# Kernel optimization log

Hardware: AMD Instinct MI355X
Metric: run time of the kernel (lower is better)

Reference implementation:

```python
import jax, jax.numpy as jnp
import numpy as np

D_MODEL = 768
N_HEADS = 12
HEAD_DIM = D_MODEL // N_HEADS


def setup_inputs() -> dict:
    key = jax.random.key(0)
    ks = jax.random.split(key, 9)
    s = 0.02
    B, S = 16, 1024
    return {
        "x": jax.random.normal(ks[0], (B, S, D_MODEL), dtype=jnp.float32),
        "Wq": jax.random.normal(ks[1], (D_MODEL, D_MODEL), dtype=jnp.float32) * s,
        "bq": jnp.zeros((D_MODEL,), dtype=jnp.float32),
        "Wk": jax.random.normal(ks[2], (D_MODEL, D_MODEL), dtype=jnp.float32) * s,
        "bk": jnp.zeros((D_MODEL,), dtype=jnp.float32),
        "Wv": jax.random.normal(ks[3], (D_MODEL, D_MODEL), dtype=jnp.float32) * s,
        "bv": jnp.zeros((D_MODEL,), dtype=jnp.float32),
        "Wc": jax.random.normal(ks[4], (D_MODEL, D_MODEL), dtype=jnp.float32) * s,
        "bc": jnpp if False else jnp.zeros((D_MODEL,), dtype=jnp.float32),
    }


def _split_heads(t):
    # [B, S, D] -> [B, H, S, Dh]
    B, S, _ = t.shape
    return t.reshape(B, S, N_HEADS, HEAD_DIM).transpose(0, 2, 1, 3)


def reference(x, Wq, bq, Wk, bk, Wv, bv, Wc, bc):
    # nn.Linear: y = x @ W.T + b ; here W stored as [out, in]-equivalent square
    q = _split_heads(x @ Wq.T + bq)
    k = _split_heads(x @ Wk.T + bk)
    v = _split_heads(x @ Wv.T + bv)
    scale = jnp.asarray(HEAD_DIM, x.dtype) ** 0.5
    scores = jnp.einsum("bhsd,bhtd->bhst", q, k) / scale  # [B,H,S,S]
    attn = jax.nn.softmax(scores, axis=-1)
    # dropout omitted (deterministic / inference-mode reference)
    ctx = jnp.einsum("bhst,bhtd->bhsd", attn, v)  # [B,H,S,Dh]
    B, H, S, Dh = ctx.shape
    ctx = ctx.transpose(0, 2, 1, 3).reshape(B, S, H * Dh)
    return ctx @ Wc.T + bc
```

## Files before the change

kernel.cpp:

```cpp
#include <hip/hip_runtime.h>
#include <hip/hip_bf16.h>
#include <stdint.h>

#define D_MODEL 768
#define NHEADS 12
#define HDIM 64
#define BATCH 16
#define SEQ 1024
#define MTOK (BATCH*SEQ)
#define LOG2E 1.4426950408889634f

typedef __bf16 bfrag  __attribute__((ext_vector_type(8)));
typedef __bf16 bf16x4 __attribute__((ext_vector_type(4)));
typedef float  f32x4  __attribute__((ext_vector_type(4)));
typedef short  s16x4  __attribute__((ext_vector_type(4)));

__device__ __forceinline__ void gload16(const void* g, void* l) {
  __builtin_amdgcn_global_load_lds(
      (const __attribute__((address_space(1))) unsigned int*)g,
      (__attribute__((address_space(3))) unsigned int*)l, 16, 0, 0);
}

__device__ __forceinline__ float fexp2(float x) {
#if __has_builtin(__builtin_amdgcn_exp2f)
  return __builtin_amdgcn_exp2f(x);
#else
  return exp2f(x);
#endif
}

__device__ __forceinline__ void mfma16(bf16x4 a, bf16x4 b, f32x4& c) {
#if __has_builtin(__builtin_amdgcn_mfma_f32_16x16x16bf16_1k)
  c = __builtin_amdgcn_mfma_f32_16x16x16bf16_1k(
        __builtin_bit_cast(s16x4, a), __builtin_bit_cast(s16x4, b), c, 0, 0, 0);
#else
  asm volatile("s_nop 1\n\tv_mfma_f32_16x16x16_bf16 %0, %1, %2, %0\n\ts_nop 7\n\ts_nop 7"
               : "+v"(c) : "v"(a), "v"(b));
#endif
}

__global__ __launch_bounds__(256) void convert_kernel(
    const float* __restrict__ x,
    const float* __restrict__ Wq, const float* __restrict__ Wk,
    const float* __restrict__ Wv, const float* __restrict__ Wc,
    __bf16* __restrict__ xb, __bf16* __restrict__ Wb)
{
  const size_t NX = (size_t)MTOK * D_MODEL;
  const size_t NW = (size_t)D_MODEL * D_MODEL;
  size_t i = ((size_t)blockIdx.x * 256 + threadIdx.x) * 4;
  const float* src; __bf16* dst; size_t off;
  if (i < NX) { src = x; dst = xb; off = i; }
  else {
    size_t wj = i - NX;
    int which = (int)(wj / NW);
    off = wj - (size_t)which * NW;
    src = which == 0 ? Wq : which == 1 ? Wk : which == 2 ? Wv : Wc;
    dst = Wb + (size_t)which * NW;
  }
  f32x4 v = *(const f32x4*)(src + off);
  bf16x4 o;
  o[0] = (__bf16)v[0]; o[1] = (__bf16)v[1]; o[2] = (__bf16)v[2]; o[3] = (__bf16)v[3];
  *(bf16x4*)(dst + off) = o;
}

__global__ __launch_bounds__(256) void qkv_gemm(
    const __bf16* __restrict__ A,
    const __bf16* __restrict__ W,
    const float* __restrict__ bq, const float* __restrict__ bk, const float* __restrict__ bv,
    __bf16* __restrict__ Qb,
    __bf16* __restrict__ Kb,
    __bf16* __restrict__ VTb)
{
  __shared__ __bf16 As[128 * 32];
  __shared__ __bf16 Bs[128 * 32];
  const int tid = threadIdx.x;
  const int lane = tid & 63, w = tid >> 6;
  const int wm = w >> 1, wn = w & 1;
  const int bm = blockIdx.x, bn = blockIdx.y;
  const int r4 = lane >> 2, c8 = (lane & 3) << 3;
  const int l15 = lane & 15, q8 = (lane >> 4) << 3;

  f32x4 acc[4][4];
#pragma unroll
  for (int mt = 0; mt < 4; ++mt)
#pragma unroll
    for (int nt = 0; nt < 4; ++nt) acc[mt][nt] = (f32x4){0.f, 0.f, 0.f, 0.f};

  const size_t am0 = (size_t)bm * 128;
  const size_t bn0 = (size_t)bn * 128;

  for (int kt = 0; kt < 24; ++kt) {
    const int k0 = kt * 32;
#pragma unroll
    for (int i = 0; i < 2; ++i) {
      const int rr = i * 64 + w * 16;
      gload16(A + (am0 + rr + r4) * D_MODEL + k0 + c8, &As[rr * 32]);
      gload16(W + (bn0 + rr + r4) * D_MODEL + k0 + c8, &Bs[rr * 32]);
    }
    __syncthreads();
    bfrag af[4], bf[4];
#pragma unroll
    for (int t = 0; t < 4; ++t) {
      af[t] = *(const bfrag*)&As[(wm * 64 + t * 16 + l15) * 32 + q8];
      bf[t] = *(const bfrag*)&Bs[(wn * 64 + t * 16 + l15) * 32 + q8];
    }
#pragma unroll
    for (int mt = 0; mt < 4; ++mt)
#pragma unroll
      for (int nt = 0; nt < 4; ++nt)
        acc[mt][nt] = __builtin_amdgcn_mfma_f32_16x16x32_bf16(af[mt], bf[nt], acc[mt][nt], 0, 0, 0);
    __syncthreads();
  }

  const int which = bn / 6;
  const int obase = (bn % 6) * 128 + wn * 64;
  const float* bias = which == 0 ? bq : which == 1 ? bk : bv;
  const float qscale = 0.125f * LOG2E;
#pragma unroll
  for (int mt = 0; mt < 4; ++mt) {
    const int row0 = bm * 128 + wm * 64 + mt * 16 + (lane >> 4) * 4;
    const int b = row0 >> 10, s = row0 & 1023;
#pragma unroll
    for (int nt = 0; nt < 4; ++nt) {
      const int o = obase + nt * 16 + l15;
      const float bo = bias[o];
      const int h = o >> 6, d = o & 63;
      const size_t hb = ((size_t)(b * NHEADS + h)) << 16;
      if (which == 2) {
        bf16x4 pv;
#pragma unroll
        for (int r = 0; r < 4; ++r) pv[r] = (__bf16)(acc[mt][nt][r] + bo);
        const int tc = s & 63;
        const size_t addr = hb + (size_t)(s >> 6) * 4096 + (size_t)d * 64
                          + (size_t)((((tc >> 3) ^ (d & 7))) << 3) + (tc & 7);
        *(bf16x4*)&VTb[addr] = pv;
      } else if (which == 0) {
#pragma unroll
        for (int r = 0; r < 4; ++r) {
          const int sr = s + r;
          const size_t addr = hb + (size_t)sr * 64 + (size_t)(((d >> 3) ^ (sr & 7)) << 3) + (d & 7);
          Qb[addr] = (__bf16)((acc[mt][nt][r] + bo) * qscale);
        }
      } else {
#pragma unroll
        for (int r = 0; r < 4; ++r) {
          const int sr = s + r;
          const size_t addr = hb + (size_t)sr * 64 + (size_t)(((d >> 3) ^ (sr & 7)) << 3) + (d & 7);
          Kb[addr] = (__bf16)(acc[mt][nt][r] + bo);
        }
      }
    }
  }
}

__global__ __launch_bounds__(256, 3) void attn_kernel(
    const __bf16* __restrict__ Qb, const __bf16* __restrict__ Kb,
    const __bf16* __restrict__ VTb, __bf16* __restrict__ ctx)
{
  __shared__ __align__(16) char smem_raw[32768];
  __shared__ float rs[256];
  __bf16* S = (__bf16*)smem_raw;
  const int tid = threadIdx.x, lane = tid & 63, w = tid >> 6;
  const int blk = blockIdx.x;
  const int xcd = blk & 7, slot = blk >> 3;
  const int bh = xcd * 24 + (slot >> 4);
  const int qt = slot & 15;
  const int l15 = lane & 15, quad = lane >> 4;
  const int h3 = l15 & 7;
  const size_t base = (size_t)bh << 16;

  const int soff = w * 1024 + lane * 8;

  {
    const __bf16* gq = Qb + base + qt * 4096 + soff;
    const __bf16* gk = Kb + base + soff;
    const __bf16* gv = VTb + base + soff;
    gload16(gq,       S + 12288 + soff);
    gload16(gq + 512, S + 12288 + soff + 512);
    gload16(gk,       S + soff);
    gload16(gk + 512, S + soff + 512);
    gload16(gv,       S + 8192 + soff);
    gload16(gv + 512, S + 8192 + soff + 512);
  }
  __syncthreads();

  bfrag bq[4][2];
#pragma unroll
  for (int q2 = 0; q2 < 4; ++q2) {
    const int fq = 12288 + (q2 * 16 + l15) * 64 + ((quad ^ h3) << 3);
    bq[q2][0] = *(const bfrag*)&S[fq];
    bq[q2][1] = *(const bfrag*)&S[fq ^ 32];
  }
  __syncthreads();

  f32x4 Oa[4][4];
#pragma unroll
  for (int dt = 0; dt < 4; ++dt)
#pragma unroll
    for (int q2 = 0; q2 < 4; ++q2) Oa[dt][q2] = (f32x4){0.f, 0.f, 0.f, 0.f};
  float sacc[4] = {0.f, 0.f, 0.f, 0.f};

  const int fk  = (w * 16 + l15) * 64 + ((quad ^ h3) << 3);
  const int fvb = l15 * 64 + (((w * 2 + (quad >> 1)) ^ h3) << 3) + ((quad & 1) << 2);

  for (int j = 0; j < 16; ++j) {
    const int cb = j & 1, nb = cb ^ 1;
    if (j < 15) {
      const __bf16* gk = Kb + base + (j + 1) * 4096 + soff;
      const __bf16* gv = VTb + base + (j + 1) * 4096 + soff;
      gload16(gk,       S + nb * 4096 + soff);
      gload16(gk + 512, S + nb * 4096 + soff + 512);
      gload16(gv,       S + 8192 + nb * 4096 + soff);
      gload16(gv + 512, S + 8192 + nb * 4096 + soff + 512);
    }
    const __bf16* Kc = S + cb * 4096;
    const __bf16* Vc = S + 8192 + cb * 4096;

    bfrag ak0 = *(const bfrag*)&Kc[fk];
    bfrag ak1 = *(const bfrag*)&Kc[fk ^ 32];
    bf16x4 av[4];
#pragma unroll
    for (int dt = 0; dt < 4; ++dt) av[dt] = *(const bf16x4*)&Vc[dt * 1024 + fvb];

    bf16x4 pb[4];
#pragma unroll
    for (int q2 = 0; q2 < 4; ++q2) {
      f32x4 s4 = (f32x4){0.f, 0.f, 0.f, 0.f};
      s4 = __builtin_amdgcn_mfma_f32_16x16x32_bf16(ak0, bq[q2][0], s4, 0, 0, 0);
      s4 = __builtin_amdgcn_mfma_f32_16x16x32_bf16(ak1, bq[q2][1], s4, 0, 0, 0);
      const float p0 = fexp2(s4[0]), p1 = fexp2(s4[1]);
      const float p2 = fexp2(s4[2]), p3 = fexp2(s4[3]);
      sacc[q2] += (p0 + p1) + (p2 + p3);
      bf16x4 pv;
      pv[0] = (__bf16)p0; pv[1] = (__bf16)p1; pv[2] = (__bf16)p2; pv[3] = (__bf16)p3;
      pb[q2] = pv;
    }

#pragma unroll
    for (int dt = 0; dt < 4; ++dt)
#pragma unroll
      for (int q2 = 0; q2 < 4; ++q2)
        mfma16(av[dt], pb[q2], Oa[dt][q2]);

    __syncthreads();
  }

  float vsum[4];
#pragma unroll
  for (int q2 = 0; q2 < 4; ++q2) {
    float v = sacc[q2];
    v += __shfl_xor(v, 16);
    v += __shfl_xor(v, 32);
    vsum[q2] = v;
  }
  if (quad == 0) {
#pragma unroll
    for (int q2 = 0; q2 < 4; ++q2) rs[w * 64 + q2 * 16 + l15] = vsum[q2];
  }
  __syncthreads();
  if (w == 0) {
    const float tot = rs[lane] + rs[64 + lane] + rs[128 + lane] + rs[192 + lane];
    rs[lane] = 1.0f / tot;
  }
  __syncthreads();

  float* fs = (float*)smem_raw;
  const int b = bh / NHEADS, h = bh - b * NHEADS;
  const int off = l15 * 16 + quad * 4;
#pragma unroll
  for (int rd = 0; rd < 2; ++rd) {
#pragma unroll
    for (int dl = 0; dl < 2; ++dl)
#pragma unroll
      for (int q2 = 0; q2 < 4; ++q2)
        *(f32x4*)&fs[w * 2048 + dl * 1024 + q2 * 256 + off] = Oa[rd * 2 + dl][q2];
    __syncthreads();
#pragma unroll
    for (int e = 0; e < 2; ++e) {
      const int idx = w * 2 + e;
      const int dl = idx >> 2, q2 = idx & 3;
      const int tb = dl * 1024 + q2 * 256 + off;
      f32x4 s0 = *(const f32x4*)&fs[tb];
      f32x4 s1 = *(const f32x4*)&fs[2048 + tb];
      f32x4 s2 = *(const f32x4*)&fs[4096 + tb];
      f32x4 s3 = *(const f32x4*)&fs[6144 + tb];
      f32x4 sum = (s0 + s1) + (s2 + s3);
      const float li = rs[q2 * 16 + l15];
      const int dt = rd * 2 + dl;
      const int s = qt * 64 + q2 * 16 + l15;
      bf16x4 o4;
#pragma unroll
      for (int r = 0; r < 4; ++r) o4[r] = (__bf16)(sum[r] * li);
      *(bf16x4*)&ctx[((size_t)(b * SEQ + s)) * D_MODEL + h * HDIM + dt * 16 + quad * 4] = o4;
    }
    __syncthreads();
  }
}

__global__ __launch_bounds__(256) void out_gemm(
    const __bf16* __restrict__ A,
    const __bf16* __restrict__ W,
    const float* __restrict__ bc,
    float* __restrict__ out)
{
  __shared__ __bf16 As[128 * 32];
  __shared__ __bf16 Bs[128 * 32];
  const int tid = threadIdx.x;
  const int lane = tid & 63, w = tid >> 6;
  const int wm = w >> 1, wn = w & 1;
  const int bm = blockIdx.x, bn = blockIdx.y;
  const int r4 = lane >> 2, c8 = (lane & 3) << 3;
  const int l15 = lane & 15, q8 = (lane >> 4) << 3;

  f32x4 acc[4][4];
#pragma unroll
  for (int mt = 0; mt < 4; ++mt)
#pragma unroll
    for (int nt = 0; nt < 4; ++nt) acc[mt][nt] = (f32x4){0.f, 0.f, 0.f, 0.f};

  const size_t am0 = (size_t)bm * 128;
  const size_t bn0 = (size_t)bn * 128;

  for (int kt = 0; kt < 24; ++kt) {
    const int k0 = kt * 32;
#pragma unroll
    for (int i = 0; i < 2; ++i) {
      const int rr = i * 64 + w * 16;
      gload16(A + (am0 + rr + r4) * D_MODEL + k0 + c8, &As[rr * 32]);
      gload16(W + (bn0 + rr + r4) * D_MODEL + k0 + c8, &Bs[rr * 32]);
    }
    __syncthreads();
    bfrag af[4], bf[4];
#pragma unroll
    for (int t = 0; t < 4; ++t) {
      af[t] = *(const bfrag*)&As[(wm * 64 + t * 16 + l15) * 32 + q8];
      bf[t] = *(const bfrag*)&Bs[(wn * 64 + t * 16 + l15) * 32 + q8];
    }
#pragma unroll
    for (int mt = 0; mt < 4; ++mt)
#pragma unroll
      for (int nt = 0; nt < 4; ++nt)
        acc[mt][nt] = __builtin_amdgcn_mfma_f32_16x16x32_bf16(af[mt], bf[nt], acc[mt][nt], 0, 0, 0);
    __syncthreads();
  }

#pragma unroll
  for (int mt = 0; mt < 4; ++mt) {
    const int row0 = bm * 128 + wm * 64 + mt * 16 + (lane >> 4) * 4;
#pragma unroll
    for (int nt = 0; nt < 4; ++nt) {
      const int o = bn * 128 + wn * 64 + nt * 16 + l15;
      const float bo = bc[o];
#pragma unroll
      for (int r = 0; r < 4; ++r)
        out[(size_t)(row0 + r) * D_MODEL + o] = acc[mt][nt][r] + bo;
    }
  }
}

extern "C" void kernel_launch(void* const* d_in, const int* in_sizes, int n_in,
                              void* d_out, int out_size, void* d_ws, size_t ws_size,
                              hipStream_t stream)
{
  const float* x  = (const float*)d_in[0];
  const float* Wq = (const float*)d_in[1];
  const float* bq = (const float*)d_in[2];
  const float* Wk = (const float*)d_in[3];
  const float* bk = (const float*)d_in[4];
  const float* Wv = (const float*)d_in[5];
  const float* bv = (const float*)d_in[6];
  const float* Wc = (const float*)d_in[7];
  const float* bc = (const float*)d_in[8];
  float* out = (float*)d_out;

  char* ws = (char*)d_ws;
  __bf16* xb  = (__bf16*)(ws);
  __bf16* Wb  = (__bf16*)(ws + 25165824);
  __bf16* Qb  = (__bf16*)(ws + 29884416);
  __bf16* Kb  = (__bf16*)(ws + 55050240);
  __bf16* VTb = (__bf16*)(ws + 80216064);
  __bf16* ctx = xb;

  convert_kernel<<<14592, 256, 0, stream>>>(x, Wq, Wk, Wv, Wc, xb, Wb);
  qkv_gemm<<<dim3(128, 18), 256, 0, stream>>>(xb, Wb, bq, bk, bv, Qb, Kb, VTb);
  attn_kernel<<<3072, 256, 0, stream>>>(Qb, Kb, VTb, ctx);
  out_gemm<<<dim3(128, 6), 256, 0, stream>>>(ctx, Wb + 3 * 589824, bc, out);
}
```

Baseline: 290.0 us.

## Rewrite projection GEMMs with 256x256 tiles and a 4-stage async LDS pipeline

```diff
diff --git a/kernel.cpp b/kernel.cpp
--- a/kernel.cpp
+++ b/kernel.cpp
@@ -63,62 +63,81 @@
   *(bf16x4*)(dst + off) = o;
 }
 
-__global__ __launch_bounds__(256) void qkv_gemm(
+__device__ __forceinline__ void gemm256_core(
+    const __bf16* __restrict__ A, const __bf16* __restrict__ Bp,
+    int am0, int bn0, __bf16* S, f32x4 (&acc)[8][4])
+{
+  const int tid = threadIdx.x;
+  const int lane = tid & 63, w = tid >> 6;
+  const int l15 = lane & 15, quad = lane >> 4;
+  const int wm = w >> 2, wn = w & 3;
+  const size_t sA0 = (size_t)(am0 + w * 16 + l15) * D_MODEL + quad * 8;
+  const size_t sA1 = sA0 + (size_t)128 * D_MODEL;
+  const size_t sB0 = (size_t)(bn0 + w * 16 + l15) * D_MODEL + quad * 8;
+  const size_t sB1 = sB0 + (size_t)128 * D_MODEL;
+  const int d0 = tid * 8, d1 = 4096 + tid * 8;
+
+#define STG(t) { __bf16* Ls = S + ((t) & 3) * 16384; const int k0 = (t) * 32; \
+    gload16(A  + sA0 + k0, Ls + d0);        \
+    gload16(A  + sA1 + k0, Ls + d1);        \
+    gload16(Bp + sB0 + k0, Ls + 8192 + d0); \
+    gload16(Bp + sB1 + k0, Ls + 8192 + d1); }
+
+#pragma unroll
+  for (int mt = 0; mt < 8; ++mt)
+#pragma unroll
+    for (int nt = 0; nt < 4; ++nt) acc[mt][nt] = (f32x4){0.f, 0.f, 0.f, 0.f};
+
+  STG(0); STG(1); STG(2);
+  asm volatile("s_waitcnt vmcnt(8)" ::: "memory");
+  __builtin_amdgcn_s_barrier();
+
+  for (int t = 0; t < 24; ++t) {
+    if (t < 21) STG(t + 3);
+    const __bf16* As_ = S + (t & 3) * 16384;
+    const __bf16* Bs_ = As_ + 8192;
+    bfrag bfr[4];
+#pragma unroll
+    for (int nt = 0; nt < 4; ++nt)
+      bfr[nt] = *(const bfrag*)&Bs_[(wn * 4 + nt) * 512 + lane * 8];
+    __builtin_amdgcn_s_setprio(1);
+#pragma unroll
+    for (int mt = 0; mt < 8; ++mt) {
+      bfrag afr = *(const bfrag*)&As_[(wm * 8 + mt) * 512 + lane * 8];
+#pragma unroll
+      for (int nt = 0; nt < 4; ++nt)
+        acc[mt][nt] = __builtin_amdgcn_mfma_f32_16x16x32_bf16(afr, bfr[nt], acc[mt][nt], 0, 0, 0);
+    }
+    __builtin_amdgcn_s_setprio(0);
+    if (t < 21)       asm volatile("s_waitcnt vmcnt(8)" ::: "memory");
+    else if (t == 21) asm volatile("s_waitcnt vmcnt(4)" ::: "memory");
+    else if (t == 22) asm volatile("s_waitcnt vmcnt(0)" ::: "memory");
+    if (t < 23) __builtin_amdgcn_s_barrier();
+  }
+#undef STG
+}
+
+__global__ __launch_bounds__(512, 2) void qkv_gemm(
     const __bf16* __restrict__ A,
     const __bf16* __restrict__ W,
     const float* __restrict__ bq, const float* __restrict__ bk, const float* __restrict__ bv,
-    __bf16* __restrict__ Qb,
-    __bf16* __restrict__ Kb,
-    __bf16* __restrict__ VTb)
-{
-  __shared__ __bf16 As[128 * 32];
-  __shared__ __bf16 Bs[128 * 32];
-  const int tid = threadIdx.x;
-  const int lane = tid & 63, w = tid >> 6;
-  const int wm = w >> 1, wn = w & 1;
-  const int bm = blockIdx.x, bn = blockIdx.y;
-  const int r4 = lane >> 2, c8 = (lane & 3) << 3;
-  const int l15 = lane & 15, q8 = (lane >> 4) << 3;
-
-  f32x4 acc[4][4];
-#pragma unroll
-  for (int mt = 0; mt < 4; ++mt)
-#pragma unroll
-    for (int nt = 0; nt < 4; ++nt) acc[mt][nt] = (f32x4){0.f, 0.f, 0.f, 0.f};
-
-  const size_t am0 = (size_t)bm * 128;
-  const size_t bn0 = (size_t)bn * 128;
-
-  for (int kt = 0; kt < 24; ++kt) {
-    const int k0 = kt * 32;
-#pragma unroll
-    for (int i = 0; i < 2; ++i) {
-      const int rr = i * 64 + w * 16;
-      gload16(A + (am0 + rr + r4) * D_MODEL + k0 + c8, &As[rr * 32]);
-      gload16(W + (bn0 + rr + r4) * D_MODEL + k0 + c8, &Bs[rr * 32]);
-    }
-    __syncthreads();
-    bfrag af[4], bf[4];
-#pragma unroll
-    for (int t = 0; t < 4; ++t) {
-      af[t] = *(const bfrag*)&As[(wm * 64 + t * 16 + l15) * 32 + q8];
-      bf[t] = *(const bfrag*)&Bs[(wn * 64 + t * 16 + l15) * 32 + q8];
-    }
-#pragma unroll
-    for (int mt = 0; mt < 4; ++mt)
-#pragma unroll
-      for (int nt = 0; nt < 4; ++nt)
-        acc[mt][nt] = __builtin_amdgcn_mfma_f32_16x16x32_bf16(af[mt], bf[nt], acc[mt][nt], 0, 0, 0);
-    __syncthreads();
-  }
-
-  const int which = bn / 6;
-  const int obase = (bn % 6) * 128 + wn * 64;
+    __bf16* __restrict__ Qb, __bf16* __restrict__ Kb, __bf16* __restrict__ VTb)
+{
+  __shared__ __bf16 S[65536];
+  f32x4 acc[8][4];
+  const int bm = blockIdx.x & 63, bn = blockIdx.x >> 6;
+  gemm256_core(A, W, bm * 256, bn * 256, S, acc);
+
+  const int tid = threadIdx.x, lane = tid & 63, w = tid >> 6;
+  const int wm = w >> 2, wn = w & 3;
+  const int l15 = lane & 15, quad = lane >> 4;
+  const int which = bn / 3;
+  const int obase = (bn % 3) * 256 + wn * 64;
   const float* bias = which == 0 ? bq : which == 1 ? bk : bv;
   const float qscale = 0.125f * LOG2E;
 #pragma unroll
-  for (int mt = 0; mt < 4; ++mt) {
-    const int row0 = bm * 128 + wm * 64 + mt * 16 + (lane >> 4) * 4;
+  for (int mt = 0; mt < 8; ++mt) {
+    const int row0 = bm * 256 + wm * 128 + mt * 16 + quad * 4;
     const int b = row0 >> 10, s = row0 & 1023;
 #pragma unroll
     for (int nt = 0; nt < 4; ++nt) {
@@ -297,59 +316,26 @@
   }
 }
 
-__global__ __launch_bounds__(256) void out_gemm(
+__global__ __launch_bounds__(512, 2) void out_gemm(
     const __bf16* __restrict__ A,
     const __bf16* __restrict__ W,
     const float* __restrict__ bc,
     float* __restrict__ out)
 {
-  __shared__ __bf16 As[128 * 32];
-  __shared__ __bf16 Bs[128 * 32];
-  const int tid = threadIdx.x;
-  const int lane = tid & 63, w = tid >> 6;
-  const int wm = w >> 1, wn = w & 1;
-  const int bm = blockIdx.x, bn = blockIdx.y;
-  const int r4 = lane >> 2, c8 = (lane & 3) << 3;
-  const int l15 = lane & 15, q8 = (lane >> 4) << 3;
-
-  f32x4 acc[4][4];
-#pragma unroll
-  for (int mt = 0; mt < 4; ++mt)
-#pragma unroll
-    for (int nt = 0; nt < 4; ++nt) acc[mt][nt] = (f32x4){0.f, 0.f, 0.f, 0.f};
-
-  const size_t am0 = (size_t)bm * 128;
-  const size_t bn0 = (size_t)bn * 128;
-
-  for (int kt = 0; kt < 24; ++kt) {
-    const int k0 = kt * 32;
-#pragma unroll
-    for (int i = 0; i < 2; ++i) {
-      const int rr = i * 64 + w * 16;
-      gload16(A + (am0 + rr + r4) * D_MODEL + k0 + c8, &As[rr * 32]);
-      gload16(W + (bn0 + rr + r4) * D_MODEL + k0 + c8, &Bs[rr * 32]);
-    }
-    __syncthreads();
-    bfrag af[4], bf[4];
-#pragma unroll
-    for (int t = 0; t < 4; ++t) {
-      af[t] = *(const bfrag*)&As[(wm * 64 + t * 16 + l15) * 32 + q8];
-      bf[t] = *(const bfrag*)&Bs[(wn * 64 + t * 16 + l15) * 32 + q8];
-    }
-#pragma unroll
-    for (int mt = 0; mt < 4; ++mt)
-#pragma unroll
-      for (int nt = 0; nt < 4; ++nt)
-        acc[mt][nt] = __builtin_amdgcn_mfma_f32_16x16x32_bf16(af[mt], bf[nt], acc[mt][nt], 0, 0, 0);
-    __syncthreads();
-  }
-
-#pragma unroll
-  for (int mt = 0; mt < 4; ++mt) {
-    const int row0 = bm * 128 + wm * 64 + mt * 16 + (lane >> 4) * 4;
+  __shared__ __bf16 S[65536];
+  f32x4 acc[8][4];
+  const int bm = blockIdx.x & 63, bn = blockIdx.x >> 6;
+  gemm256_core(A, W, bm * 256, bn * 256, S, acc);
+
+  const int tid = threadIdx.x, lane = tid & 63, w = tid >> 6;
+  const int wm = w >> 2, wn = w & 3;
+  const int l15 = lane & 15, quad = lane >> 4;
+#pragma unroll
+  for (int mt = 0; mt < 8; ++mt) {
+    const int row0 = bm * 256 + wm * 128 + mt * 16 + quad * 4;
 #pragma unroll
     for (int nt = 0; nt < 4; ++nt) {
-      const int o = bn * 128 + wn * 64 + nt * 16 + l15;
+      const int o = bn * 256 + wn * 64 + nt * 16 + l15;
       const float bo = bc[o];
 #pragma unroll
       for (int r = 0; r < 4; ++r)
@@ -382,7 +368,7 @@
   __bf16* ctx = xb;
 
   convert_kernel<<<14592, 256, 0, stream>>>(x, Wq, Wk, Wv, Wc, xb, Wb);
-  qkv_gemm<<<dim3(128, 18), 256, 0, stream>>>(xb, Wb, bq, bk, bv, Qb, Kb, VTb);
+  qkv_gemm<<<576, 512, 0, stream>>>(xb, Wb, bq, bk, bv, Qb, Kb, VTb);
   attn_kernel<<<3072, 256, 0, stream>>>(Qb, Kb, VTb, ctx);
-  out_gemm<<<dim3(128, 6), 256, 0, stream>>>(ctx, Wb + 3 * 589824, bc, out);
-}
+  out_gemm<<<192, 512, 0, stream>>>(ctx, Wb + 3 * 589824, bc, out);
+}
```

Result: slower. 304.5 us (+5.0%).

## Process 128-key K/V tiles per attention iteration with larger LDS buffers

Applied to the files above, without the earlier changes.

```diff
diff --git a/kernel.cpp b/kernel.cpp
--- a/kernel.cpp
+++ b/kernel.cpp
@@ -67,9 +67,7 @@
     const __bf16* __restrict__ A,
     const __bf16* __restrict__ W,
     const float* __restrict__ bq, const float* __restrict__ bk, const float* __restrict__ bv,
-    __bf16* __restrict__ Qb,
-    __bf16* __restrict__ Kb,
-    __bf16* __restrict__ VTb)
+    __bf16* __restrict__ Qb, __bf16* __restrict__ Kb, __bf16* __restrict__ VTb)
 {
   __shared__ __bf16 As[128 * 32];
   __shared__ __bf16 Bs[128 * 32];
@@ -153,11 +151,11 @@
   }
 }
 
-__global__ __launch_bounds__(256, 3) void attn_kernel(
+__global__ __launch_bounds__(256, 2) void attn_kernel(
     const __bf16* __restrict__ Qb, const __bf16* __restrict__ Kb,
     const __bf16* __restrict__ VTb, __bf16* __restrict__ ctx)
 {
-  __shared__ __align__(16) char smem_raw[32768];
+  __shared__ __align__(16) char smem_raw[65536];
   __shared__ float rs[256];
   __bf16* S = (__bf16*)smem_raw;
   const int tid = threadIdx.x, lane = tid & 63, w = tid >> 6;
@@ -169,25 +167,27 @@
   const int h3 = l15 & 7;
   const size_t base = (size_t)bh << 16;
 
-  const int soff = w * 1024 + lane * 8;
+  const int soff  = w * 1024 + lane * 8;
+  const int soff2 = w * 2048 + lane * 8;
 
   {
     const __bf16* gq = Qb + base + qt * 4096 + soff;
-    const __bf16* gk = Kb + base + soff;
-    const __bf16* gv = VTb + base + soff;
-    gload16(gq,       S + 12288 + soff);
-    gload16(gq + 512, S + 12288 + soff + 512);
-    gload16(gk,       S + soff);
-    gload16(gk + 512, S + soff + 512);
-    gload16(gv,       S + 8192 + soff);
-    gload16(gv + 512, S + 8192 + soff + 512);
+    gload16(gq,       S + 24576 + soff);
+    gload16(gq + 512, S + 24576 + soff + 512);
+    const __bf16* gk = Kb + base + soff2;
+    const __bf16* gv = VTb + base + soff2;
+#pragma unroll
+    for (int c = 0; c < 4; ++c) {
+      gload16(gk + c * 512, S + soff2 + c * 512);
+      gload16(gv + c * 512, S + 16384 + soff2 + c * 512);
+    }
   }
   __syncthreads();
 
   bfrag bq[4][2];
 #pragma unroll
   for (int q2 = 0; q2 < 4; ++q2) {
-    const int fq = 12288 + (q2 * 16 + l15) * 64 + ((quad ^ h3) << 3);
+    const int fq = 24576 + (q2 * 16 + l15) * 64 + ((quad ^ h3) << 3);
     bq[q2][0] = *(const bfrag*)&S[fq];
     bq[q2][1] = *(const bfrag*)&S[fq ^ 32];
   }
@@ -200,47 +200,53 @@
     for (int q2 = 0; q2 < 4; ++q2) Oa[dt][q2] = (f32x4){0.f, 0.f, 0.f, 0.f};
   float sacc[4] = {0.f, 0.f, 0.f, 0.f};
 
-  const int fk  = (w * 16 + l15) * 64 + ((quad ^ h3) << 3);
-  const int fvb = l15 * 64 + (((w * 2 + (quad >> 1)) ^ h3) << 3) + ((quad & 1) << 2);
-
-  for (int j = 0; j < 16; ++j) {
+  for (int j = 0; j < 8; ++j) {
     const int cb = j & 1, nb = cb ^ 1;
-    if (j < 15) {
-      const __bf16* gk = Kb + base + (j + 1) * 4096 + soff;
-      const __bf16* gv = VTb + base + (j + 1) * 4096 + soff;
-      gload16(gk,       S + nb * 4096 + soff);
-      gload16(gk + 512, S + nb * 4096 + soff + 512);
-      gload16(gv,       S + 8192 + nb * 4096 + soff);
-      gload16(gv + 512, S + 8192 + nb * 4096 + soff + 512);
-    }
-    const __bf16* Kc = S + cb * 4096;
-    const __bf16* Vc = S + 8192 + cb * 4096;
-
-    bfrag ak0 = *(const bfrag*)&Kc[fk];
-    bfrag ak1 = *(const bfrag*)&Kc[fk ^ 32];
-    bf16x4 av[4];
-#pragma unroll
-    for (int dt = 0; dt < 4; ++dt) av[dt] = *(const bf16x4*)&Vc[dt * 1024 + fvb];
-
-    bf16x4 pb[4];
-#pragma unroll
-    for (int q2 = 0; q2 < 4; ++q2) {
-      f32x4 s4 = (f32x4){0.f, 0.f, 0.f, 0.f};
-      s4 = __builtin_amdgcn_mfma_f32_16x16x32_bf16(ak0, bq[q2][0], s4, 0, 0, 0);
-      s4 = __builtin_amdgcn_mfma_f32_16x16x32_bf16(ak1, bq[q2][1], s4, 0, 0, 0);
-      const float p0 = fexp2(s4[0]), p1 = fexp2(s4[1]);
-      const float p2 = fexp2(s4[2]), p3 = fexp2(s4[3]);
-      sacc[q2] += (p0 + p1) + (p2 + p3);
-      bf16x4 pv;
-      pv[0] = (__bf16)p0; pv[1] = (__bf16)p1; pv[2] = (__bf16)p2; pv[3] = (__bf16)p3;
-      pb[q2] = pv;
-    }
-
-#pragma unroll
-    for (int dt = 0; dt < 4; ++dt)
-#pragma unroll
-      for (int q2 = 0; q2 < 4; ++q2)
-        mfma16(av[dt], pb[q2], Oa[dt][q2]);
+    if (j < 7) {
+      const __bf16* gk = Kb + base + (j + 1) * 8192 + soff2;
+      const __bf16* gv = VTb + base + (j + 1) * 8192 + soff2;
+#pragma unroll
+      for (int c = 0; c < 4; ++c) {
+        gload16(gk + c * 512, S + nb * 8192 + soff2 + c * 512);
+        gload16(gv + c * 512, S + 16384 + nb * 8192 + soff2 + c * 512);
+      }
+    }
+    const __bf16* Kc = S + cb * 8192;
+    const __bf16* Vc = S + 16384 + cb * 8192;
+
+#pragma unroll
+    for (int g = 0; g < 2; ++g) {
+      const int tb = w * 32 + g * 16;
+      const int fk = (tb + l15) * 64 + ((quad ^ h3) << 3);
+      bfrag ak0 = *(const bfrag*)&Kc[fk];
+      bfrag ak1 = *(const bfrag*)&Kc[fk ^ 32];
+      const int fvb = (w >> 1) * 4096 + l15 * 64
+                    + ((((w & 1) * 4 + g * 2 + (quad >> 1)) ^ h3) << 3)
+                    + ((quad & 1) << 2);
+      bf16x4 av[4];
+#pragma unroll
+      for (int dt = 0; dt < 4; ++dt) av[dt] = *(const bf16x4*)&Vc[fvb + dt * 1024];
+
+      bf16x4 pb[4];
+#pragma unroll
+      for (int q2 = 0; q2 < 4; ++q2) {
+        f32x4 s4 = (f32x4){0.f, 0.f, 0.f, 0.f};
+        s4 = __builtin_amdgcn_mfma_f32_16x16x32_bf16(ak0, bq[q2][0], s4, 0, 0, 0);
+        s4 = __builtin_amdgcn_mfma_f32_16x16x32_bf16(ak1, bq[q2][1], s4, 0, 0, 0);
+        const float p0 = fexp2(s4[0]), p1 = fexp2(s4[1]);
+        const float p2 = fexp2(s4[2]), p3 = fexp2(s4[3]);
+        sacc[q2] += (p0 + p1) + (p2 + p3);
+        bf16x4 pv;
+        pv[0] = (__bf16)p0; pv[1] = (__bf16)p1; pv[2] = (__bf16)p2; pv[3] = (__bf16)p3;
+        pb[q2] = pv;
+      }
+
+#pragma unroll
+      for (int dt = 0; dt < 4; ++dt)
+#pragma unroll
+        for (int q2 = 0; q2 < 4; ++q2)
+          mfma16(av[dt], pb[q2], Oa[dt][q2]);
+    }
 
     __syncthreads();
   }
@@ -279,11 +285,11 @@
     for (int e = 0; e < 2; ++e) {
       const int idx = w * 2 + e;
       const int dl = idx >> 2, q2 = idx & 3;
-      const int tb = dl * 1024 + q2 * 256 + off;
-      f32x4 s0 = *(const f32x4*)&fs[tb];
-      f32x4 s1 = *(const f32x4*)&fs[2048 + tb];
-      f32x4 s2 = *(const f32x4*)&fs[4096 + tb];
-      f32x4 s3 = *(const f32x4*)&fs[6144 + tb];
+      const int tb2 = dl * 1024 + q2 * 256 + off;
+      f32x4 s0 = *(const f32x4*)&fs[tb2];
+      f32x4 s1 = *(const f32x4*)&fs[2048 + tb2];
+      f32x4 s2 = *(const f32x4*)&fs[4096 + tb2];
+      f32x4 s3 = *(const f32x4*)&fs[6144 + tb2];
       f32x4 sum = (s0 + s1) + (s2 + s3);
       const float li = rs[q2 * 16 + l15];
       const int dt = rd * 2 + dl;
```

Result: slower. 303.0 us (+4.5%).

## Deepen GEMM K-tile to 64 with XOR-swizzled LDS and pad attention reduction

Applied to the files above, without the earlier changes.

```diff
diff --git a/kernel.cpp b/kernel.cpp
--- a/kernel.cpp
+++ b/kernel.cpp
@@ -63,22 +63,23 @@
   *(bf16x4*)(dst + off) = o;
 }
 
+
 __global__ __launch_bounds__(256) void qkv_gemm(
     const __bf16* __restrict__ A,
     const __bf16* __restrict__ W,
     const float* __restrict__ bq, const float* __restrict__ bk, const float* __restrict__ bv,
-    __bf16* __restrict__ Qb,
-    __bf16* __restrict__ Kb,
-    __bf16* __restrict__ VTb)
+    __bf16* __restrict__ Qb, __bf16* __restrict__ Kb, __bf16* __restrict__ VTb)
 {
-  __shared__ __bf16 As[128 * 32];
-  __shared__ __bf16 Bs[128 * 32];
+  __shared__ __bf16 As[128 * 64];
+  __shared__ __bf16 Bs[128 * 64];
   const int tid = threadIdx.x;
   const int lane = tid & 63, w = tid >> 6;
   const int wm = w >> 1, wn = w & 1;
   const int bm = blockIdx.x, bn = blockIdx.y;
-  const int r4 = lane >> 2, c8 = (lane & 3) << 3;
-  const int l15 = lane & 15, q8 = (lane >> 4) << 3;
+  const int l15 = lane & 15, quad = lane >> 4;
+  const int h3 = l15 & 7;
+  const int srow = lane >> 3;
+  const int cu8 = ((lane & 7) ^ srow) << 3;
 
   f32x4 acc[4][4];
 #pragma unroll
@@ -89,26 +90,32 @@
   const size_t am0 = (size_t)bm * 128;
   const size_t bn0 = (size_t)bn * 128;
 
-  for (int kt = 0; kt < 24; ++kt) {
-    const int k0 = kt * 32;
-#pragma unroll
-    for (int i = 0; i < 2; ++i) {
-      const int rr = i * 64 + w * 16;
-      gload16(A + (am0 + rr + r4) * D_MODEL + k0 + c8, &As[rr * 32]);
-      gload16(W + (bn0 + rr + r4) * D_MODEL + k0 + c8, &Bs[rr * 32]);
-    }
-    __syncthreads();
-    bfrag af[4], bf[4];
+  for (int kt = 0; kt < 12; ++kt) {
+    const int k0 = kt * 64;
+#pragma unroll
+    for (int i = 0; i < 4; ++i) {
+      const int row = i * 32 + w * 8 + srow;
+      gload16(A + (am0 + row) * D_MODEL + k0 + cu8, &As[(i * 32 + w * 8) * 64 + lane * 8]);
+      gload16(W + (bn0 + row) * D_MODEL + k0 + cu8, &Bs[(i * 32 + w * 8) * 64 + lane * 8]);
+    }
+    __syncthreads();
+    bfrag af[4][2], bf[4][2];
 #pragma unroll
     for (int t = 0; t < 4; ++t) {
-      af[t] = *(const bfrag*)&As[(wm * 64 + t * 16 + l15) * 32 + q8];
-      bf[t] = *(const bfrag*)&Bs[(wn * 64 + t * 16 + l15) * 32 + q8];
+      const int ra = (wm * 64 + t * 16 + l15) * 64 + ((quad ^ h3) << 3);
+      const int rb = (wn * 64 + t * 16 + l15) * 64 + ((quad ^ h3) << 3);
+      af[t][0] = *(const bfrag*)&As[ra];
+      af[t][1] = *(const bfrag*)&As[ra ^ 32];
+      bf[t][0] = *(const bfrag*)&Bs[rb];
+      bf[t][1] = *(const bfrag*)&Bs[rb ^ 32];
     }
 #pragma unroll
     for (int mt = 0; mt < 4; ++mt)
 #pragma unroll
-      for (int nt = 0; nt < 4; ++nt)
-        acc[mt][nt] = __builtin_amdgcn_mfma_f32_16x16x32_bf16(af[mt], bf[nt], acc[mt][nt], 0, 0, 0);
+      for (int nt = 0; nt < 4; ++nt) {
+        acc[mt][nt] = __builtin_amdgcn_mfma_f32_16x16x32_bf16(af[mt][0], bf[nt][0], acc[mt][nt], 0, 0, 0);
+        acc[mt][nt] = __builtin_amdgcn_mfma_f32_16x16x32_bf16(af[mt][1], bf[nt][1], acc[mt][nt], 0, 0, 0);
+      }
     __syncthreads();
   }
 
@@ -118,7 +125,7 @@
   const float qscale = 0.125f * LOG2E;
 #pragma unroll
   for (int mt = 0; mt < 4; ++mt) {
-    const int row0 = bm * 128 + wm * 64 + mt * 16 + (lane >> 4) * 4;
+    const int row0 = bm * 128 + wm * 64 + mt * 16 + quad * 4;
     const int b = row0 >> 10, s = row0 & 1023;
 #pragma unroll
     for (int nt = 0; nt < 4; ++nt) {
@@ -153,11 +160,11 @@
   }
 }
 
-__global__ __launch_bounds__(256, 3) void attn_kernel(
+__global__ __launch_bounds__(256, 4) void attn_kernel(
     const __bf16* __restrict__ Qb, const __bf16* __restrict__ Kb,
     const __bf16* __restrict__ VTb, __bf16* __restrict__ ctx)
 {
-  __shared__ __align__(16) char smem_raw[32768];
+  __shared__ __align__(16) char smem_raw[34816];
   __shared__ float rs[256];
   __bf16* S = (__bf16*)smem_raw;
   const int tid = threadIdx.x, lane = tid & 63, w = tid >> 6;
@@ -266,31 +273,32 @@
 
   float* fs = (float*)smem_raw;
   const int b = bh / NHEADS, h = bh - b * NHEADS;
-  const int off = l15 * 16 + quad * 4;
+  const int off = l15 * 17 + quad * 4;
 #pragma unroll
   for (int rd = 0; rd < 2; ++rd) {
 #pragma unroll
     for (int dl = 0; dl < 2; ++dl)
 #pragma unroll
-      for (int q2 = 0; q2 < 4; ++q2)
-        *(f32x4*)&fs[w * 2048 + dl * 1024 + q2 * 256 + off] = Oa[rd * 2 + dl][q2];
+      for (int q2 = 0; q2 < 4; ++q2) {
+        float* p = &fs[w * 2176 + dl * 1088 + q2 * 272 + off];
+        const f32x4 v = Oa[rd * 2 + dl][q2];
+        p[0] = v[0]; p[1] = v[1]; p[2] = v[2]; p[3] = v[3];
+      }
     __syncthreads();
 #pragma unroll
     for (int e = 0; e < 2; ++e) {
       const int idx = w * 2 + e;
       const int dl = idx >> 2, q2 = idx & 3;
-      const int tb = dl * 1024 + q2 * 256 + off;
-      f32x4 s0 = *(const f32x4*)&fs[tb];
-      f32x4 s1 = *(const f32x4*)&fs[2048 + tb];
-      f32x4 s2 = *(const f32x4*)&fs[4096 + tb];
-      f32x4 s3 = *(const f32x4*)&fs[6144 + tb];
-      f32x4 sum = (s0 + s1) + (s2 + s3);
+      const int tb = dl * 1088 + q2 * 272 + off;
       const float li = rs[q2 * 16 + l15];
       const int dt = rd * 2 + dl;
       const int s = qt * 64 + q2 * 16 + l15;
       bf16x4 o4;
 #pragma unroll
-      for (int r = 0; r < 4; ++r) o4[r] = (__bf16)(sum[r] * li);
+      for (int r = 0; r < 4; ++r) {
+        const float sum = (fs[tb + r] + fs[2176 + tb + r]) + (fs[4352 + tb + r] + fs[6528 + tb + r]);
+        o4[r] = (__bf16)(sum * li);
+      }
       *(bf16x4*)&ctx[((size_t)(b * SEQ + s)) * D_MODEL + h * HDIM + dt * 16 + quad * 4] = o4;
     }
     __syncthreads();
@@ -303,14 +311,16 @@
     const float* __restrict__ bc,
     float* __restrict__ out)
 {
-  __shared__ __bf16 As[128 * 32];
-  __shared__ __bf16 Bs[128 * 32];
+  __shared__ __bf16 As[128 * 64];
+  __shared__ __bf16 Bs[128 * 64];
   const int tid = threadIdx.x;
   const int lane = tid & 63, w = tid >> 6;
   const int wm = w >> 1, wn = w & 1;
   const int bm = blockIdx.x, bn = blockIdx.y;
-  const int r4 = lane >> 2, c8 = (lane & 3) << 3;
-  const int l15 = lane & 15, q8 = (lane >> 4) << 3;
+  const int l15 = lane & 15, quad = lane >> 4;
+  const int h3 = l15 & 7;
+  const int srow = lane >> 3;
+  const int cu8 = ((lane & 7) ^ srow) << 3;
 
   f32x4 acc[4][4];
 #pragma unroll
@@ -321,32 +331,38 @@
   const size_t am0 = (size_t)bm * 128;
   const size_t bn0 = (size_t)bn * 128;
 
-  for (int kt = 0; kt < 24; ++kt) {
-    const int k0 = kt * 32;
-#pragma unroll
-    for (int i = 0; i < 2; ++i) {
-      const int rr = i * 64 + w * 16;
-      gload16(A + (am0 + rr + r4) * D_MODEL + k0 + c8, &As[rr * 32]);
-      gload16(W + (bn0 + rr + r4) * D_MODEL + k0 + c8, &Bs[rr * 32]);
-    }
-    __syncthreads();
-    bfrag af[4], bf[4];
+  for (int kt = 0; kt < 12; ++kt) {
+    const int k0 = kt * 64;
+#pragma unroll
+    for (int i = 0; i < 4; ++i) {
+      const int row = i * 32 + w * 8 + srow;
+      gload16(A + (am0 + row) * D_MODEL + k0 + cu8, &As[(i * 32 + w * 8) * 64 + lane * 8]);
+      gload16(W + (bn0 + row) * D_MODEL + k0 + cu8, &Bs[(i * 32 + w * 8) * 64 + lane * 8]);
+    }
+    __syncthreads();
+    bfrag af[4][2], bf[4][2];
 #pragma unroll
     for (int t = 0; t < 4; ++t) {
-      af[t] = *(const bfrag*)&As[(wm * 64 + t * 16 + l15) * 32 + q8];
-      bf[t] = *(const bfrag*)&Bs[(wn * 64 + t * 16 + l15) * 32 + q8];
+      const int ra = (wm * 64 + t * 16 + l15) * 64 + ((quad ^ h3) << 3);
+      const int rb = (wn * 64 + t * 16 + l15) * 64 + ((quad ^ h3) << 3);
+      af[t][0] = *(const bfrag*)&As[ra];
+      af[t][1] = *(const bfrag*)&As[ra ^ 32];
+      bf[t][0] = *(const bfrag*)&Bs[rb];
+      bf[t][1] = *(const bfrag*)&Bs[rb ^ 32];
     }
 #pragma unroll
     for (int mt = 0; mt < 4; ++mt)
 #pragma unroll
-      for (int nt = 0; nt < 4; ++nt)
-        acc[mt][nt] = __builtin_amdgcn_mfma_f32_16x16x32_bf16(af[mt], bf[nt], acc[mt][nt], 0, 0, 0);
+      for (int nt = 0; nt < 4; ++nt) {
+        acc[mt][nt] = __builtin_amdgcn_mfma_f32_16x16x32_bf16(af[mt][0], bf[nt][0], acc[mt][nt], 0, 0, 0);
+        acc[mt][nt] = __builtin_amdgcn_mfma_f32_16x16x32_bf16(af[mt][1], bf[nt][1], acc[mt][nt], 0, 0, 0);
+      }
     __syncthreads();
   }
 
 #pragma unroll
   for (int mt = 0; mt < 4; ++mt) {
-    const int row0 = bm * 128 + wm * 64 + mt * 16 + (lane >> 4) * 4;
+    const int row0 = bm * 128 + wm * 64 + mt * 16 + quad * 4;
 #pragma unroll
     for (int nt = 0; nt < 4; ++nt) {
       const int o = bn * 128 + wn * 64 + nt * 16 + l15;
```

Measured after the change: 596.3 us. 2.06x slower.
